# Optimization experiments

Measured on AMD Instinct MI355X. Metric: run time of the kernel, lower is better.

The kernel has to match this reference:

```python
import jax, jax.numpy as jnp
import numpy as np


def rel_to_abs(x):
    """[b, hh, L, 2L-1] -> [b, hh, L, L] via pad/reshape trick."""
    b, hh, L, _ = x.shape
    x = jnp.pad(x, ((0, 0), (0, 0), (0, 0), (0, 1)))          # [b,hh,L,2L]
    flat = x.reshape(b, hh, L * 2 * L)
    flat = jnp.pad(flat, ((0, 0), (0, 0), (0, L - 1)))
    final = flat.reshape(b, hh, L + 1, 2 * L - 1)
    return final[:, :, :L, L - 1:]                             # [b,hh,L,L]


def relative_logits_1d(q, rel_k, transpose_mask):
    # q: [b, n, x, y, d]; rel_k: [2y-1, d]
    b, n, x, y, d = q.shape
    rel = jnp.einsum('bnxyd,md->bnxym', q, rel_k)
    rel = rel.reshape(b, n * x, y, 2 * y - 1)
    rel = rel_to_abs(rel)                                      # [b, n*x, y, y]
    rel = rel.reshape(b, n, x, y, y)
    rel = jnp.broadcast_to(rel[:, :, :, None, :, :], (b, n, x, x, y, y))
    return jnp.transpose(rel, transpose_mask)


def relative_logits(q, rel_emb_w, rel_emb_h):
    logits_w = relative_logits_1d(q, rel_emb_w, (0, 1, 2, 4, 3, 5))
    q_t = jnp.transpose(q, (0, 1, 3, 2, 4))  # swap h/w
    logits_h = relative_logits_1d(q_t, rel_emb_h, (0, 1, 4, 2, 5, 3))
    return logits_h + logits_w  # [b,n,h,w,h,w]


def setup_inputs() -> dict:
    key = jax.random.key(0)
    k1, k2, k3, k4, k5 = jax.random.split(key, 5)
    B, N, H, W, D = 4, 4, 48, 48, 32
    std = D ** (-0.5)
    return {
        'q': jax.random.normal(k1, (B, N, H, W, D), jnp.float32),
        'k': jax.random.normal(k2, (B, N, H, W, D), jnp.float32),
        'v': jax.random.normal(k3, (B, N, H, W, D), jnp.float32),
        'rel_emb_w': jax.random.normal(k4, (2 * W - 1, D), jnp.float32) * std,
        'rel_emb_h': jax.random.normal(k5, (2 * H - 1, D), jnp.float32) * std,
    }


def reference(q, k, v, rel_emb_w, rel_emb_h):
    bs, heads, h, w, dim = q.shape
    q = q * dim ** (-0.5)
    logits = jnp.einsum('bnhwd,bnpqd->bnhwpq', q, k)
    logits = logits + relative_logits(q, rel_emb_w, rel_emb_h)
    weights = jax.nn.softmax(logits.reshape(bs, heads, h, w, h * w), axis=-1)
    weights = weights.reshape(bs, heads, h, w, h, w)
    attn_out = jnp.einsum('bnhwpq,bnpqd->bhwnd', weights, v)
    # fold_heads=True
    return attn_out.reshape(bs, h, w, heads * dim)
```

## Files before the change

kernel.cpp:

```cpp
#include <hip/hip_runtime.h>
#include <hip/hip_bf16.h>


typedef __attribute__((ext_vector_type(8))) short bf16x8;
typedef __attribute__((ext_vector_type(4))) float f32x4;

#define DEVFN __device__ __forceinline__
#define AS1 __attribute__((address_space(1)))
#define AS3 __attribute__((address_space(3)))

#if __has_builtin(__builtin_amdgcn_exp2f)
#define EXP2(x) __builtin_amdgcn_exp2f(x)
#else
#define EXP2(x) exp2f(x)
#endif

constexpr int H_ = 48, W_ = 48, D_ = 32;
constexpr int L_ = H_ * W_;
constexpr int BN_ = 16;

constexpr int QB2 = 48;
constexpr int KB2 = 96;
constexpr int IT2 = L_ / KB2;
constexpr int QT2 = L_ / QB2;
constexpr int NWG2 = BN_ * QT2;

constexpr size_t WE_Q = 0;
constexpr size_t WE_K = 1179648;
constexpr size_t WE_V = 2359296;
constexpr size_t WE_R = 3538944;
constexpr size_t WS_NEED = (WE_R + 2 * 6 * 64 * 8) * 2;

DEVFN unsigned short f2bf(float f) {
  unsigned u = __float_as_uint(f);
  return (unsigned short)((u + 0x7fffu + ((u >> 16) & 1u)) >> 16);
}
DEVFN unsigned pk2(float lo, float hi) {
  return (unsigned)f2bf(lo) | ((unsigned)f2bf(hi) << 16);
}
DEVFN unsigned pkcvt(float lo, float hi) {
  __hip_bfloat162 h = __float22bfloat162_rn(make_float2(lo, hi));
  union { __hip_bfloat162 h2; unsigned u; } cv; cv.h2 = h;
  return cv.u;
}
DEVFN void llds16(void* l, const void* g) {
  __builtin_amdgcn_global_load_lds((const AS1 unsigned*)g, (AS3 unsigned*)l, 16, 0, 0);
}

template <int CTRL>
DEVFN float dppf(float x) {
  return __int_as_float(__builtin_amdgcn_update_dpp(0, __float_as_int(x), CTRL, 0xF, 0xF, true));
}
DEVFN float rowmax16(float x) {
  x = fmaxf(x, dppf<0x128>(x));
  x = fmaxf(x, dppf<0x124>(x));
  x = fmaxf(x, dppf<0x122>(x));
  x = fmaxf(x, dppf<0x121>(x));
  return x;
}
DEVFN float rowsum16(float x) {
  x += dppf<0x128>(x);
  x += dppf<0x124>(x);
  x += dppf<0x122>(x);
  x += dppf<0x121>(x);
  return x;
}

__global__ __launch_bounds__(256)
void prep_kernel(const float* __restrict__ Q, const float* __restrict__ K,
                 const float* __restrict__ V, const float* __restrict__ RW,
                 const float* __restrict__ RH, unsigned short* __restrict__ ws)
{
  __shared__ __align__(16) float Vl[3072];
  const int bid = blockIdx.x, tid = threadIdx.x;
  const float QS = 0.17677669529663687f * 1.4426950408889634f;
  if (bid < 576) {
    size_t e = ((size_t)bid * 256 + tid) * 8;
    const float* s = Q + e;
    float4 a = *(const float4*)s, c = *(const float4*)(s + 4);
    uint4 wv;
    wv.x = pkcvt(a.x * QS, a.y * QS); wv.y = pkcvt(a.z * QS, a.w * QS);
    wv.z = pkcvt(c.x * QS, c.y * QS); wv.w = pkcvt(c.z * QS, c.w * QS);
    *(uint4*)(ws + WE_Q + e) = wv;
  } else if (bid < 1152) {
    int idx = (bid - 576) * 256 + tid;
    int lane = idx & 63, t = idx >> 6;
    int l15 = lane & 15, lg = lane >> 4;
    int bn = t / 144, t16 = t % 144;
    int it = t16 / 6, kb = t16 % 6;
    int kbp = kb >> 1, f = kb & 1;
    int key96 = kbp * 32 + (l15 >> 2) * 8 + f * 4 + (l15 & 3);
    const float* s = K + ((size_t)(bn * L_ + it * 96 + key96) * D_ + lg * 8);
    float4 a = *(const float4*)s, c = *(const float4*)(s + 4);
    uint4 wv;
    wv.x = pkcvt(a.x, a.y); wv.y = pkcvt(a.z, a.w);
    wv.z = pkcvt(c.x, c.y); wv.w = pkcvt(c.z, c.w);
    *(uint4*)(ws + WE_K + (size_t)idx * 8) = wv;
  } else if (bid < 1536) {
    const int tile = bid - 1152;
    const float* src = V + (size_t)tile * 96 * D_;
    #pragma unroll
    for (int u = 0; u < 3; ++u)
      ((float4*)Vl)[tid + u * 256] = ((const float4*)src)[tid + u * 256];
    __syncthreads();
    unsigned short* dst = ws + WE_V + (size_t)tile * 3072;
    #pragma unroll
    for (int u = 0; u < 2; ++u) {
      const int f2i = tid + u * 256;
      if (f2i < 384) {
        const int f2 = f2i >> 6, lane = f2i & 63;
        const int l15 = lane & 15, lg = lane >> 4;
        const int kbp = f2 >> 1, half = f2 & 1;
        const int d = half * 16 + l15;
        float fv[8];
        #pragma unroll
        for (int j = 0; j < 8; ++j)
          fv[j] = Vl[(kbp * 32 + lg * 8 + j) * 32 + d];
        uint4 wv;
        wv.x = pkcvt(fv[0], fv[1]); wv.y = pkcvt(fv[2], fv[3]);
        wv.z = pkcvt(fv[4], fv[5]); wv.w = pkcvt(fv[6], fv[7]);
        *(uint4*)(dst + (size_t)f2i * 8) = wv;
      }
    }
  } else {
    int t = (bid - 1536) * 256 + tid;
    if (t < 768) {
      int tbl = t / 384, rem = t % 384, jb = rem / 64, lane = rem % 64;
      int l15 = lane & 15, lg = lane >> 4;
      int j = jb * 16 + l15;
      int jc = (j > 94) ? 94 : j;
      const float* s = (tbl ? RW : RH) + jc * D_ + lg * 8;
      float4 a = *(const float4*)s, c = *(const float4*)(s + 4);
      uint4 wv;
      wv.x = pkcvt(a.x, a.y); wv.y = pkcvt(a.z, a.w);
      wv.z = pkcvt(c.x, c.y); wv.w = pkcvt(c.z, c.w);
      *(uint4*)(ws + WE_R + (size_t)t * 8) = wv;
    }
  }
}

__global__ __launch_bounds__(192, 2)
void relattn3(const unsigned short* __restrict__ ws, float* __restrict__ OUT)
{
  __shared__ __align__(16) char lds[34176];
  unsigned short* Kbase = (unsigned short*)lds;
  unsigned short* Vbase = (unsigned short*)(lds + 12288);
  float* BhT = (float*)(lds + 24576);
  float* BwT = (float*)lds;

  const unsigned short* Qb = ws + WE_Q;
  const unsigned short* Kf = ws + WE_K;
  const unsigned short* Vf = ws + WE_V;
  const unsigned short* Rf = ws + WE_R;

  const int bid = blockIdx.x;
  const int wg  = (bid & 7) * (NWG2 / 8) + (bid >> 3);
  const int bn  = wg / QT2;
  const int qb  = (wg % QT2) * QB2;
  const int b   = bn >> 2, n = bn & 3;

  const int tid  = threadIdx.x;
  const int wave = tid >> 6;
  const int lane = tid & 63;
  const int l15  = lane & 15;
  const int lg   = lane >> 4;

  const int qi = qb + wave * 16 + l15;
  const bf16x8 qfrag = *(const bf16x8*)(Qb + (size_t)(bn * L_ + qi) * D_ + lg * 8);

  const f32x4 z4 = {0.f, 0.f, 0.f, 0.f};

  int hq[4], wq[4];
  #pragma unroll
  for (int r = 0; r < 4; ++r) {
    int qg = qb + wave * 16 + lg * 4 + r;
    hq[r] = qg / 48; wq[r] = qg % 48;
  }

  #pragma unroll
  for (int jb = 0; jb < 6; ++jb) {
    bf16x8 rhf = *(const bf16x8*)(Rf + ((0 * 6 + jb) * 64 + lane) * 8);
    bf16x8 rwf = *(const bf16x8*)(Rf + ((1 * 6 + jb) * 64 + lane) * 8);
    f32x4 mh = __builtin_amdgcn_mfma_f32_16x16x32_bf16(qfrag, rhf, z4, 0, 0, 0);
    f32x4 mw = __builtin_amdgcn_mfma_f32_16x16x32_bf16(qfrag, rwf, z4, 0, 0, 0);
    const int j = jb * 16 + l15;
    if (j < 95) {
      #pragma unroll
      for (int r = 0; r < 4; ++r) {
        const int row = wave * 16 + lg * 4 + r;
        const int p  = j - 47 + hq[r];
        if (p >= 0 && p < 48)  BhT[row * 50 + p]  = mh[r];
        const int ww = j - 47 + wq[r];
        if (ww >= 0 && ww < 48) BwT[row * 52 + ww] = mw[r];
      }
    }
  }

  const int q52 = (wave * 16 + l15) * 52;
  const int bt0 = lg * 8;
  const int bt1 = (lg < 2) ? (lg * 8 + 32) : (lg * 8 - 16);
  const int bt2 = lg * 8 + 16;
  float bwv[3][8];
  *(float4*)&bwv[0][0] = *(const float4*)&BwT[q52 + bt0];
  *(float4*)&bwv[0][4] = *(const float4*)&BwT[q52 + bt0 + 4];
  *(float4*)&bwv[1][0] = *(const float4*)&BwT[q52 + bt1];
  *(float4*)&bwv[1][4] = *(const float4*)&BwT[q52 + bt1 + 4];
  *(float4*)&bwv[2][0] = *(const float4*)&BwT[q52 + bt2];
  *(float4*)&bwv[2][4] = *(const float4*)&BwT[q52 + bt2 + 4];

  __syncthreads();

  const unsigned short* KfB = Kf + (size_t)bn * 24 * 3072;
  const unsigned short* VfB = Vf + (size_t)bn * 24 * 3072;

  auto stage = [&](int buf, int it) {
    const unsigned short* kt = KfB + (size_t)it * 3072;
    const unsigned short* vt = VfB + (size_t)it * 3072;
    char* kd = lds + buf * 6144;
    char* vd = lds + 12288 + buf * 6144;
    #pragma unroll
    for (int g2 = 0; g2 < 4; ++g2) {
      const int g = wave * 4 + g2;
      if (g < 6) llds16(kd + g * 1024, kt + g * 512 + lane * 8);
      else       llds16(vd + (g - 6) * 1024, vt + (g - 6) * 512 + lane * 8);
    }
  };

  f32x4 acc0 = z4, acc1 = z4;
  float l_acc = 0.f;

  const float* bhrow = &BhT[(wave * 16 + l15) * 50];
  const bool lglo = (lg < 2);

  stage(0, 0);
  __syncthreads();
  int cur = 0;

  for (int it = 0; it < IT2; ++it) {
    if (it + 1 < IT2) stage(cur ^ 1, it + 1);

    const unsigned short* kb_ = Kbase + cur * 3072;
    const unsigned short* vb_ = Vbase + cur * 3072;

    const float2 bh2 = *(const float2*)(bhrow + it * 2);
    const float bhm = lglo ? bh2.x : bh2.y;

    #pragma unroll
    for (int kbp = 0; kbp < 3; ++kbp) {
      const float bhsel = (kbp == 0) ? bh2.x : ((kbp == 2) ? bh2.y : bhm);
      f32x4 cin0, cin1;
      #pragma unroll
      for (int r = 0; r < 4; ++r) {
        cin0[r] = bhsel + bwv[kbp][r];
        cin1[r] = bhsel + bwv[kbp][4 + r];
      }
      bf16x8 kf0 = *(const bf16x8*)(kb_ + ((kbp * 2 + 0) * 64 + lane) * 8);
      bf16x8 kf1 = *(const bf16x8*)(kb_ + ((kbp * 2 + 1) * 64 + lane) * 8);
      f32x4 s0 = __builtin_amdgcn_mfma_f32_16x16x32_bf16(kf0, qfrag, cin0, 0, 0, 0);
      f32x4 s1 = __builtin_amdgcn_mfma_f32_16x16x32_bf16(kf1, qfrag, cin1, 0, 0, 0);

      const float e0 = EXP2(s0[0]), e1 = EXP2(s0[1]), e2 = EXP2(s0[2]), e3 = EXP2(s0[3]);
      const float e4 = EXP2(s1[0]), e5 = EXP2(s1[1]), e6 = EXP2(s1[2]), e7 = EXP2(s1[3]);
      l_acc += (((e0 + e1) + (e2 + e3)) + ((e4 + e5) + (e6 + e7)));
      union { unsigned u[4]; bf16x8 v; } pf;
      pf.u[0] = pkcvt(e0, e1); pf.u[1] = pkcvt(e2, e3);
      pf.u[2] = pkcvt(e4, e5); pf.u[3] = pkcvt(e6, e7);

      bf16x8 vf0 = *(const bf16x8*)(vb_ + ((kbp * 2 + 0) * 64 + lane) * 8);
      bf16x8 vf1 = *(const bf16x8*)(vb_ + ((kbp * 2 + 1) * 64 + lane) * 8);
      acc0 = __builtin_amdgcn_mfma_f32_16x16x32_bf16(vf0, pf.v, acc0, 0, 0, 0);
      acc1 = __builtin_amdgcn_mfma_f32_16x16x32_bf16(vf1, pf.v, acc1, 0, 0, 0);
    }

    __syncthreads();
    cur ^= 1;
  }

  float ls = l_acc;
  ls += __shfl_xor(ls, 16);
  ls += __shfl_xor(ls, 32);
  const float inv = __builtin_amdgcn_rcpf(ls);
  const int ql = qb + wave * 16 + l15;
  const int hql = ql / 48, wql = ql % 48;
  float* op = OUT + ((size_t)(b * 48 + hql) * 48 + wql) * 128 + n * 32 + lg * 4;
  *(float4*)op        = make_float4(acc0[0] * inv, acc0[1] * inv, acc0[2] * inv, acc0[3] * inv);
  *(float4*)(op + 16) = make_float4(acc1[0] * inv, acc1[1] * inv, acc1[2] * inv, acc1[3] * inv);
}

__global__ __launch_bounds__(256, 2)
void relattn_kernel(const float* __restrict__ Q, const float* __restrict__ K,
                    const float* __restrict__ V, const float* __restrict__ RW,
                    const float* __restrict__ RH, float* __restrict__ OUT)
{
  __shared__ __align__(16) unsigned short Klds[64][40];
  __shared__ __align__(16) unsigned       VT[32][36];
  __shared__ __align__(16) unsigned short Plds[4][16][72];
  __shared__ __align__(16) float          Bh[64][49];
  __shared__ __align__(16) float          Bw[64][49];

  const int bid = blockIdx.x;
  const int wg  = (bid & 7) * 72 + (bid >> 3);
  const int bn  = wg / 36;
  const int qb  = (wg % 36) * 64;
  const int b   = bn >> 2, n = bn & 3;

  const int tid  = threadIdx.x;
  const int wave = tid >> 6;
  const int lane = tid & 63;
  const int l15  = lane & 15;
  const int lg   = lane >> 4;

  const float QS = 0.17677669529663687f * 1.4426950408889634f;
  const int qi = qb + wave * 16 + l15;
  bf16x8 qfrag;
  {
    const float* qr = Q + ((bn * L_ + qi) * D_ + lg * 8);
    float4 a = *(const float4*)qr;
    float4 c = *(const float4*)(qr + 4);
    qfrag[0] = (short)f2bf(a.x * QS); qfrag[1] = (short)f2bf(a.y * QS);
    qfrag[2] = (short)f2bf(a.z * QS); qfrag[3] = (short)f2bf(a.w * QS);
    qfrag[4] = (short)f2bf(c.x * QS); qfrag[5] = (short)f2bf(c.y * QS);
    qfrag[6] = (short)f2bf(c.z * QS); qfrag[7] = (short)f2bf(c.w * QS);
  }
  const f32x4 z4 = {0.f, 0.f, 0.f, 0.f};
  #pragma unroll
  for (int jb = 0; jb < 6; ++jb) {
    const int j  = jb * 16 + l15;
    const int jc = (j > 94) ? 94 : j;
    bf16x8 rhf, rwf;
    {
      const float* rr = RH + jc * D_ + lg * 8;
      float4 a = *(const float4*)rr; float4 c = *(const float4*)(rr + 4);
      rhf[0] = (short)f2bf(a.x); rhf[1] = (short)f2bf(a.y);
      rhf[2] = (short)f2bf(a.z); rhf[3] = (short)f2bf(a.w);
      rhf[4] = (short)f2bf(c.x); rhf[5] = (short)f2bf(c.y);
      rhf[6] = (short)f2bf(c.z); rhf[7] = (short)f2bf(c.w);
      const float* rr2 = RW + jc * D_ + lg * 8;
      float4 a2 = *(const float4*)rr2; float4 c2 = *(const float4*)(rr2 + 4);
      rwf[0] = (short)f2bf(a2.x); rwf[1] = (short)f2bf(a2.y);
      rwf[2] = (short)f2bf(a2.z); rwf[3] = (short)f2bf(a2.w);
      rwf[4] = (short)f2bf(c2.x); rwf[5] = (short)f2bf(c2.y);
      rwf[6] = (short)f2bf(c2.z); rwf[7] = (short)f2bf(c2.w);
    }
    f32x4 mh = __builtin_amdgcn_mfma_f32_16x16x32_bf16(qfrag, rhf, z4, 0, 0, 0);
    f32x4 mw = __builtin_amdgcn_mfma_f32_16x16x32_bf16(qfrag, rwf, z4, 0, 0, 0);
    #pragma unroll
    for (int r = 0; r < 4; ++r) {
      const int qrow = lg * 4 + r;
      const int qg   = qb + wave * 16 + qrow;
      const int hqv  = qg / 48, wqv = qg % 48;
      if (j < 95) {
        const int p  = j - 47 + hqv;
        if (p >= 0 && p < 48) Bh[wave * 16 + qrow][p] = mh[r];
        const int ww = j - 47 + wqv;
        if (ww >= 0 && ww < 48) Bw[wave * 16 + qrow][ww] = mw[r];
      }
    }
  }
  float bw0[4], bw1[4], bw2[4];
  #pragma unroll
  for (int r = 0; r < 4; ++r) {
    bw0[r] = Bw[wave * 16 + lg * 4 + r][ 0 + l15];
    bw1[r] = Bw[wave * 16 + lg * 4 + r][16 + l15];
    bw2[r] = Bw[wave * 16 + lg * 4 + r][32 + l15];
  }
  f32x4 acc0 = z4, acc1 = z4;
  float m_r[4] = {-INFINITY, -INFINITY, -INFINITY, -INFINITY};
  float l_r[4] = {0.f, 0.f, 0.f, 0.f};
  const float* kbase = K + bn * L_ * D_;
  const float* vbase = V + bn * L_ * D_;
  for (int it = 0; it < 36; ++it) {
    const int kv0 = it * 64;
    __syncthreads();
    {
      const int r = tid >> 2, c = (tid & 3) * 8;
      const float* s = kbase + (kv0 + r) * D_ + c;
      float4 a = *(const float4*)s; float4 cc = *(const float4*)(s + 4);
      uint4 wv;
      wv.x = pk2(a.x, a.y);  wv.y = pk2(a.z, a.w);
      wv.z = pk2(cc.x, cc.y); wv.w = pk2(cc.z, cc.w);
      *(uint4*)&Klds[r][c] = wv;
    }
    {
      const int kp = tid >> 3, dg = tid & 7;
      const float* s0 = vbase + (kv0 + 2 * kp) * D_ + dg * 4;
      float4 a = *(const float4*)s0;
      float4 c = *(const float4*)(s0 + D_);
      VT[dg * 4 + 0][kp] = pk2(a.x, c.x);
      VT[dg * 4 + 1][kp] = pk2(a.y, c.y);
      VT[dg * 4 + 2][kp] = pk2(a.z, c.z);
      VT[dg * 4 + 3][kp] = pk2(a.w, c.w);
    }
    __syncthreads();
    f32x4 sacc[4];
    #pragma unroll
    for (int kb = 0; kb < 4; ++kb) {
      bf16x8 kf = *(const bf16x8*)&Klds[kb * 16 + l15][lg * 8];
      sacc[kb] = __builtin_amdgcn_mfma_f32_16x16x32_bf16(qfrag, kf, z4, 0, 0, 0);
    }
    const int p0   = kv0 / 48;
    const int tthr = (p0 + 1) * 48 - kv0;
    const int m0   = it % 3;
    float bh0[4], bh1[4];
    #pragma unroll
    for (int r = 0; r < 4; ++r) {
      bh0[r] = Bh[wave * 16 + lg * 4 + r][p0];
      bh1[r] = Bh[wave * 16 + lg * 4 + r][p0 + 1];
    }
    #pragma unroll
    for (int kb = 0; kb < 4; ++kb) {
      const bool hi = (kb * 16 + l15) >= tthr;
      int mm = m0 + kb; if (mm >= 3) mm -= 3; if (mm >= 3) mm -= 3;
      #pragma unroll
      for (int r = 0; r < 4; ++r) {
        const float bwv2 = (mm == 0) ? bw0[r] : ((mm == 1) ? bw1[r] : bw2[r]);
        sacc[kb][r] += (hi ? bh1[r] : bh0[r]) + bwv2;
      }
    }
    #pragma unroll
    for (int r = 0; r < 4; ++r) {
      float mx = fmaxf(fmaxf(sacc[0][r], sacc[1][r]), fmaxf(sacc[2][r], sacc[3][r]));
      mx = rowmax16(mx);
      const float mn = fmaxf(m_r[r], mx);
      const float sc = exp2f(m_r[r] - mn);
      m_r[r] = mn;
      acc0[r] *= sc; acc1[r] *= sc;
      const float pe0 = exp2f(sacc[0][r] - mn);
      const float pe1 = exp2f(sacc[1][r] - mn);
      const float pe2 = exp2f(sacc[2][r] - mn);
      const float pe3 = exp2f(sacc[3][r] - mn);
      const float rs = rowsum16(pe0 + pe1 + pe2 + pe3);
      l_r[r] = l_r[r] * sc + rs;
      const int prow = lg * 4 + r;
      Plds[wave][prow][ 0 + l15] = f2bf(pe0);
      Plds[wave][prow][16 + l15] = f2bf(pe1);
      Plds[wave][prow][32 + l15] = f2bf(pe2);
      Plds[wave][prow][48 + l15] = f2bf(pe3);
    }
    const unsigned short* VTu = (const unsigned short*)VT;
    #pragma unroll
    for (int s2 = 0; s2 < 2; ++s2) {
      bf16x8 a2 = *(const bf16x8*)&Plds[wave][l15][s2 * 32 + lg * 8];
      bf16x8 b0 = *(const bf16x8*)&VTu[( 0 + l15) * 72 + s2 * 32 + lg * 8];
      bf16x8 b1 = *(const bf16x8*)&VTu[(16 + l15) * 72 + s2 * 32 + lg * 8];
      acc0 = __builtin_amdgcn_mfma_f32_16x16x32_bf16(a2, b0, acc0, 0, 0, 0);
      acc1 = __builtin_amdgcn_mfma_f32_16x16x32_bf16(a2, b1, acc1, 0, 0, 0);
    }
  }
  #pragma unroll
  for (int r = 0; r < 4; ++r) {
    const int qg = qb + wave * 16 + lg * 4 + r;
    const int hqv = qg / 48, wqv = qg % 48;
    const float inv = __builtin_amdgcn_rcpf(l_r[r]);
    float* op = OUT + ((b * 48 + hqv) * 48 + wqv) * 128 + n * 32 + l15;
    op[0]  = acc0[r] * inv;
    op[16] = acc1[r] * inv;
  }
}

extern "C" void kernel_launch(void* const* d_in, const int* in_sizes, int n_in,
                              void* d_out, int out_size, void* d_ws, size_t ws_size,
                              hipStream_t stream) {
  const float* q  = (const float*)d_in[0];
  const float* k  = (const float*)d_in[1];
  const float* v  = (const float*)d_in[2];
  const float* rw = (const float*)d_in[3];
  const float* rh = (const float*)d_in[4];
  float* out = (float*)d_out;
  if (ws_size >= WS_NEED) {
    unsigned short* ws = (unsigned short*)d_ws;
    hipLaunchKernelGGL(prep_kernel, dim3(1539), dim3(256), 0, stream, q, k, v, rw, rh, ws);
    hipLaunchKernelGGL(relattn3, dim3(NWG2), dim3(192), 0, stream, ws, out);
  } else {
    hipLaunchKernelGGL(relattn_kernel, dim3(576), dim3(256), 0, stream, q, k, v, rw, rh, out);
  }
}
```

Measured before the change: 46.79 us.

## Load K/V fragments directly from global into registers, drop LDS double buffering

Replaces the LDS double-buffered K/V staging (global_load_lds plus a barrier each iteration) with per-wave direct global loads of the pre-swizzled bf16 K/V fragments into registers. Each of the three waves now reads the full K/V tile independently, relying on L1/L2 to absorb the redundancy. This removes the per-iteration __syncthreads and LDS traffic, and shrinks LDS to the bias tables, which may allow more workgroups per CU. In exchange it triples global/L2 read traffic for K/V, holds the fragments in more registers, and loses explicit prefetch of the next tile, so load latency may be exposed.

```diff
diff --git a/kernel.cpp b/kernel.cpp
--- a/kernel.cpp
+++ b/kernel.cpp
@@ -6,8 +6,6 @@
 typedef __attribute__((ext_vector_type(4))) float f32x4;
 
 #define DEVFN __device__ __forceinline__
-#define AS1 __attribute__((address_space(1)))
-#define AS3 __attribute__((address_space(3)))
 
 #if __has_builtin(__builtin_amdgcn_exp2f)
 #define EXP2(x) __builtin_amdgcn_exp2f(x)
@@ -42,9 +40,6 @@
   __hip_bfloat162 h = __float22bfloat162_rn(make_float2(lo, hi));
   union { __hip_bfloat162 h2; unsigned u; } cv; cv.h2 = h;
   return cv.u;
-}
-DEVFN void llds16(void* l, const void* g) {
-  __builtin_amdgcn_global_load_lds((const AS1 unsigned*)g, (AS3 unsigned*)l, 16, 0, 0);
 }
 
 template <int CTRL>
@@ -140,13 +135,10 @@
 }
 
 __global__ __launch_bounds__(192, 2)
-void relattn3(const unsigned short* __restrict__ ws, float* __restrict__ OUT)
+void relattn4(const unsigned short* __restrict__ ws, float* __restrict__ OUT)
 {
-  __shared__ __align__(16) char lds[34176];
-  unsigned short* Kbase = (unsigned short*)lds;
-  unsigned short* Vbase = (unsigned short*)(lds + 12288);
-  float* BhT = (float*)(lds + 24576);
-  float* BwT = (float*)lds;
+  __shared__ __align__(16) float BhT[48 * 50];
+  __shared__ __align__(16) float BwT[48 * 52];
 
   const unsigned short* Qb = ws + WE_Q;
   const unsigned short* Kf = ws + WE_K;
@@ -208,39 +200,23 @@
   *(float4*)&bwv[2][0] = *(const float4*)&BwT[q52 + bt2];
   *(float4*)&bwv[2][4] = *(const float4*)&BwT[q52 + bt2 + 4];
 
-  __syncthreads();
-
-  const unsigned short* KfB = Kf + (size_t)bn * 24 * 3072;
-  const unsigned short* VfB = Vf + (size_t)bn * 24 * 3072;
-
-  auto stage = [&](int buf, int it) {
+  const unsigned short* KfB = Kf + (size_t)bn * 24 * 3072 + (size_t)lane * 8;
+  const unsigned short* VfB = Vf + (size_t)bn * 24 * 3072 + (size_t)lane * 8;
+
+  f32x4 acc0 = z4, acc1 = z4;
+  float l_acc = 0.f;
+
+  const float* bhrow = &BhT[(wave * 16 + l15) * 50];
+  const bool lglo = (lg < 2);
+
+  for (int it = 0; it < IT2; ++it) {
     const unsigned short* kt = KfB + (size_t)it * 3072;
     const unsigned short* vt = VfB + (size_t)it * 3072;
-    char* kd = lds + buf * 6144;
-    char* vd = lds + 12288 + buf * 6144;
-    #pragma unroll
-    for (int g2 = 0; g2 < 4; ++g2) {
-      const int g = wave * 4 + g2;
-      if (g < 6) llds16(kd + g * 1024, kt + g * 512 + lane * 8);
-      else       llds16(vd + (g - 6) * 1024, vt + (g - 6) * 512 + lane * 8);
-    }
-  };
-
-  f32x4 acc0 = z4, acc1 = z4;
-  float l_acc = 0.f;
-
-  const float* bhrow = &BhT[(wave * 16 + l15) * 50];
-  const bool lglo = (lg < 2);
-
-  stage(0, 0);
-  __syncthreads();
-  int cur = 0;
-
-  for (int it = 0; it < IT2; ++it) {
-    if (it + 1 < IT2) stage(cur ^ 1, it + 1);
-
-    const unsigned short* kb_ = Kbase + cur * 3072;
-    const unsigned short* vb_ = Vbase + cur * 3072;
+    bf16x8 kf[6], vf[6];
+    #pragma unroll
+    for (int u = 0; u < 6; ++u) kf[u] = *(const bf16x8*)(kt + u * 512);
+    #pragma unroll
+    for (int u = 0; u < 6; ++u) vf[u] = *(const bf16x8*)(vt + u * 512);
 
     const float2 bh2 = *(const float2*)(bhrow + it * 2);
     const float bhm = lglo ? bh2.x : bh2.y;
@@ -254,10 +230,8 @@
         cin0[r] = bhsel + bwv[kbp][r];
         cin1[r] = bhsel + bwv[kbp][4 + r];
       }
-      bf16x8 kf0 = *(const bf16x8*)(kb_ + ((kbp * 2 + 0) * 64 + lane) * 8);
-      bf16x8 kf1 = *(const bf16x8*)(kb_ + ((kbp * 2 + 1) * 64 + lane) * 8);
-      f32x4 s0 = __builtin_amdgcn_mfma_f32_16x16x32_bf16(kf0, qfrag, cin0, 0, 0, 0);
-      f32x4 s1 = __builtin_amdgcn_mfma_f32_16x16x32_bf16(kf1, qfrag, cin1, 0, 0, 0);
+      f32x4 s0 = __builtin_amdgcn_mfma_f32_16x16x32_bf16(kf[kbp * 2 + 0], qfrag, cin0, 0, 0, 0);
+      f32x4 s1 = __builtin_amdgcn_mfma_f32_16x16x32_bf16(kf[kbp * 2 + 1], qfrag, cin1, 0, 0, 0);
 
       const float e0 = EXP2(s0[0]), e1 = EXP2(s0[1]), e2 = EXP2(s0[2]), e3 = EXP2(s0[3]);
       const float e4 = EXP2(s1[0]), e5 = EXP2(s1[1]), e6 = EXP2(s1[2]), e7 = EXP2(s1[3]);
@@ -266,14 +240,9 @@
       pf.u[0] = pkcvt(e0, e1); pf.u[1] = pkcvt(e2, e3);
       pf.u[2] = pkcvt(e4, e5); pf.u[3] = pkcvt(e6, e7);
 
-      bf16x8 vf0 = *(const bf16x8*)(vb_ + ((kbp * 2 + 0) * 64 + lane) * 8);
-      bf16x8 vf1 = *(const bf16x8*)(vb_ + ((kbp * 2 + 1) * 64 + lane) * 8);
-      acc0 = __builtin_amdgcn_mfma_f32_16x16x32_bf16(vf0, pf.v, acc0, 0, 0, 0);
-      acc1 = __builtin_amdgcn_mfma_f32_16x16x32_bf16(vf1, pf.v, acc1, 0, 0, 0);
-    }
-
-    __syncthreads();
-    cur ^= 1;
+      acc0 = __builtin_amdgcn_mfma_f32_16x16x32_bf16(vf[kbp * 2 + 0], pf.v, acc0, 0, 0, 0);
+      acc1 = __builtin_amdgcn_mfma_f32_16x16x32_bf16(vf[kbp * 2 + 1], pf.v, acc1, 0, 0, 0);
+    }
   }
 
   float ls = l_acc;
@@ -470,7 +439,7 @@
   if (ws_size >= WS_NEED) {
     unsigned short* ws = (unsigned short*)d_ws;
     hipLaunchKernelGGL(prep_kernel, dim3(1539), dim3(256), 0, stream, q, k, v, rw, rh, ws);
-    hipLaunchKernelGGL(relattn3, dim3(NWG2), dim3(192), 0, stream, ws, out);
+    hipLaunchKernelGGL(relattn4, dim3(NWG2), dim3(192), 0, stream, ws, out);
   } else {
     hipLaunchKernelGGL(relattn_kernel, dim3(576), dim3(256), 0, stream, q, k, v, rw, rh, out);
   }
```

Result: slower. 50.60 us (+8.2%).
